# Optimization experiments

Hardware: AMD Instinct MI355X
Metric: run time of the kernel (lower is better)

The kernel has to match this reference:

```python
import jax, jax.numpy as jnp
import numpy as np

N = 50000      # nodes
E = 800000     # edges
DIN = 256
DH = 256
DOUT = 64


def setup_inputs() -> dict:
    key = jax.random.key(0)
    ks = jax.random.split(key, 8)
    x = jax.random.normal(ks[0], (N, DIN), dtype=jnp.float32)
    edge_index = jax.random.randint(ks[1], (2, E), 0, N, dtype=jnp.int64)
    s = 0.05
    W1 = jax.random.normal(ks[2], (DIN, DH), dtype=jnp.float32) * s
    b1 = jnp.zeros((DH,), dtype=jnp.float32)
    W2 = jax.random.normal(ks[3], (DH, DH), dtype=jnp.float32) * s
    b2 = jnp.zeros((DH,), dtype=jnp.float32)
    W3 = jax.random.normal(ks[4], (DH, DOUT), dtype=jnp.float32) * s
    b3 = jnp.zeros((DOUT,), dtype=jnp.float32)
    return {"x": x, "edge_index": edge_index, "W1": W1, "b1": b1,
            "W2": W2, "b2": b2, "W3": W3, "b3": b3}


def gcn_conv(x, src, dst, deg_inv_sqrt, W, b):
    # x: [N, din] -> [N, dout]. PyG GCNConv: h = D^{-1/2}(A+I)D^{-1/2} (x W) + b
    n = x.shape[0]
    h = x @ W                                   # [N, dout]
    norm = deg_inv_sqrt[src] * deg_inv_sqrt[dst]  # [E+N]
    msgs = h[src] * norm[:, None]               # gather + scale, [E+N, dout]
    out = jax.ops.segment_sum(msgs, dst, num_segments=n)  # scatter-add
    return out + b


def _loops(edge_index, n):
    # add self loops, compute symmetric normalization degrees
    sl = jnp.arange(n, dtype=edge_index.dtype)
    src = jnp.concatenate([edge_index[0], sl])
    dst = jnp.concatenate([edge_index[1], sl])
    deg = jax.ops.segment_sum(jnp.ones_like(dst, dtype=jnp.float32), dst, num_segments=n)
    dis = jnp.where(deg > 0, jax.lax.rsqrt(deg), 0.0)
    return src, dst, dis


def reference(x, edge_index, W1, b1, W2, b2, W3, b3):
    src, dst, dis = _loops(edge_index, x.shape[0])
    h = jax.nn.relu(gcn_conv(x, src, dst, dis, W1, b1))   # dropout: eval no-op
    h = jax.nn.relu(gcn_conv(h, src, dst, dis, W2, b2))
    out = gcn_conv(h, src, dst, dis, W3, b3)              # batch=None -> no pooling
    return out
```

## Files before the change

kernel.cpp:

```cpp
#include <hip/hip_runtime.h>
#include <cstdint>
#include <cstddef>

typedef unsigned short u16;
typedef _Float16 f16x8 __attribute__((ext_vector_type(8)));
typedef _Float16 h2 __attribute__((ext_vector_type(2)));
typedef float f32x4 __attribute__((ext_vector_type(4)));

__device__ __forceinline__ float h2f(u16 u) {
  return (float)__builtin_bit_cast(_Float16, u);
}
__device__ __forceinline__ u16 f2h(float f) {
  return __builtin_bit_cast(u16, (_Float16)f);
}

__device__ __forceinline__ void async16(u16* lds, const u16* g) {
  __builtin_amdgcn_global_load_lds(
      (const __attribute__((address_space(1))) unsigned int*)g,
      (__attribute__((address_space(3))) unsigned int*)lds, 16, 0, 0);
}

__device__ __forceinline__ void fma8(float* a, float d, uint4 p) {
  a[0] += d * h2f((u16)p.x); a[1] += d * h2f((u16)(p.x >> 16));
  a[2] += d * h2f((u16)p.y); a[3] += d * h2f((u16)(p.y >> 16));
  a[4] += d * h2f((u16)p.z); a[5] += d * h2f((u16)(p.z >> 16));
  a[6] += d * h2f((u16)p.w); a[7] += d * h2f((u16)(p.w >> 16));
}

__device__ __forceinline__ void pkfma4(h2* acc, h2 w, uint4 p) {
  acc[0] += __builtin_bit_cast(h2, p.x) * w;
  acc[1] += __builtin_bit_cast(h2, p.y) * w;
  acc[2] += __builtin_bit_cast(h2, p.z) * w;
  acc[3] += __builtin_bit_cast(h2, p.w) * w;
}

__device__ __forceinline__ int wave_is64(const void* ep) {
  const unsigned* p = (const unsigned*)ep;
  const int lane = threadIdx.x & 63;
  unsigned v = p[2 * lane + 1] | p[2 * (lane + 64) + 1];
  unsigned long long bal = __ballot(v != 0u);
  return (bal == 0ull) ? 1 : 0;
}

__device__ __forceinline__ int edge_at(const void* ep, int is64, long long idx) {
  if (is64) return (int)((const long long*)ep)[idx];
  return ((const int*)ep)[idx];
}

__global__ void zero_f32(float* p, int n) {
  int i = blockIdx.x * 256 + threadIdx.x;
  if (i < n) p[i] = 0.f;
}

__global__ __launch_bounds__(256) void prep_fused(
    const float4* __restrict__ x, ushort4* __restrict__ xpad, int n_src4, int n_tot4,
    const float* __restrict__ W1, u16* __restrict__ wt1,
    const float* __restrict__ W2, u16* __restrict__ wt2,
    const float* __restrict__ W3, u16* __restrict__ wt3,
    int DIN, int DH, int DOUT,
    int nb_cvt, int nb_w1, int nb_w2) {
  int b = blockIdx.x;
  if (b < nb_cvt) {
    int i = b * 256 + threadIdx.x;
    if (i < n_tot4) {
      ushort4 o = {0, 0, 0, 0};
      if (i < n_src4) {
        float4 v = x[i];
        o.x = f2h(v.x); o.y = f2h(v.y); o.z = f2h(v.z); o.w = f2h(v.w);
      }
      xpad[i] = o;
    }
    return;
  }
  b -= nb_cvt;
  if (b < nb_w1) {
    int idx = b * 256 + threadIdx.x;
    if (idx < DIN * DH) {
      int n = idx / DIN, k = idx % DIN;
      wt1[idx] = f2h(W1[k * DH + n]);
    }
    return;
  }
  b -= nb_w1;
  if (b < nb_w2) {
    int idx = b * 256 + threadIdx.x;
    if (idx < DH * DH) {
      int n = idx / DH, k = idx % DH;
      wt2[idx] = f2h(W2[k * DH + n]);
    }
    return;
  }
  b -= nb_w2;
  {
    int idx = b * 256 + threadIdx.x;
    if (idx < DH * DOUT) {
      int n = idx / DH, k = idx % DH;
      wt3[idx] = f2h(W3[k * DOUT + n]);
    }
  }
}

#define NCHUNK 64

__global__ __launch_bounds__(256) void csr_hist(const void* __restrict__ ep,
                                                int* __restrict__ cnt, int E, int N) {
  __shared__ int h[256];
  h[threadIdx.x] = 0;
  __syncthreads();
  int is64 = wave_is64(ep);
  const int chunk = blockIdx.x;
  const int per = (E + NCHUNK - 1) / NCHUNK;
  const int e0 = chunk * per, e1 = min(e0 + per, E);
  for (int e = e0 + threadIdx.x; e < e1; e += 256) {
    int d = edge_at(ep, is64, (long long)E + e);
    d = min(max(d, 0), N - 1);
    atomicAdd(&h[d >> 8], 1);
  }
  __syncthreads();
  cnt[threadIdx.x * NCHUNK + chunk] = h[threadIdx.x];
}

__global__ __launch_bounds__(256) void csr_base(const int* __restrict__ cnt,
                                                int* __restrict__ bases,
                                                int* __restrict__ off,
                                                int nbuck, int E) {
  __shared__ int ws4[8];
  const int t = threadIdx.x, lane = t & 63, w = t >> 6;
  int tot = 0;
  if (t < nbuck)
#pragma unroll 8
    for (int c = 0; c < NCHUNK; ++c) tot += cnt[t * NCHUNK + c];
  int inc = tot;
#pragma unroll
  for (int o = 1; o < 64; o <<= 1) {
    int u = __shfl_up(inc, o, 64);
    if (lane >= o) inc += u;
  }
  if (lane == 63) ws4[w] = inc;
  __syncthreads();
  if (t == 0) {
    int run = 0;
#pragma unroll
    for (int k = 0; k < 4; ++k) { int v = ws4[k]; ws4[k + 4] = run; run += v; }
  }
  __syncthreads();
  const int base = ws4[w + 4] + inc - tot;
  if (t < nbuck) {
    bases[t] = base;
    int run = base;
    for (int c = 0; c < NCHUNK; ++c) {
      off[t * NCHUNK + c] = run;
      run += cnt[t * NCHUNK + c];
    }
  }
  if (t == 0) bases[nbuck] = E;
}

__global__ __launch_bounds__(256) void csr_bucket(const void* __restrict__ ep,
                                                  const int* __restrict__ off,
                                                  unsigned* __restrict__ tmp,
                                                  int E, int N) {
  __shared__ int cur[256];
  const int chunk = blockIdx.x;
  const int nbuck = (N + 255) >> 8;
  if ((int)threadIdx.x < nbuck) cur[threadIdx.x] = off[threadIdx.x * NCHUNK + chunk];
  __syncthreads();
  int is64 = wave_is64(ep);
  const int per = (E + NCHUNK - 1) / NCHUNK;
  const int e0 = chunk * per, e1 = min(e0 + per, E);
  for (int e = e0 + threadIdx.x; e < e1; e += 256) {
    int s = edge_at(ep, is64, e);
    int d = edge_at(ep, is64, (long long)E + e);
    s = min(max(s, 0), N - 1);
    d = min(max(d, 0), N - 1);
    int pos = atomicAdd(&cur[d >> 8], 1);
    tmp[pos] = ((unsigned)d << 16) | (unsigned)s;
  }
}

__global__ __launch_bounds__(256) void csr_final(const unsigned* __restrict__ tmp,
                                                 const int* __restrict__ bases,
                                                 int* __restrict__ rp,
                                                 float* __restrict__ dis,
                                                 u16* __restrict__ col, int N, int E) {
  __shared__ int hcnt[256];
  __shared__ int curs[256];
  __shared__ int ws4[8];
  const int b = blockIdx.x;
  const int node0 = b * 256;
  const int t = threadIdx.x, lane = t & 63, w = t >> 6;
  hcnt[t] = 0;
  __syncthreads();
  const int k0 = bases[b];
  const int k1 = bases[b + 1];
  for (int k = k0 + t; k < k1; k += 256)
    atomicAdd(&hcnt[(int)(tmp[k] >> 16) - node0], 1);
  __syncthreads();
  const int v = hcnt[t];
  int inc = v;
#pragma unroll
  for (int o = 1; o < 64; o <<= 1) {
    int u = __shfl_up(inc, o, 64);
    if (lane >= o) inc += u;
  }
  if (lane == 63) ws4[w] = inc;
  __syncthreads();
  if (t == 0) {
    int run = 0;
#pragma unroll
    for (int k = 0; k < 4; ++k) { int vv = ws4[k]; ws4[k + 4] = run; run += vv; }
  }
  __syncthreads();
  const int excl = k0 + ws4[w + 4] + inc - v;
  if (node0 + t < N) {
    rp[node0 + t] = excl;
    dis[node0 + t] = rsqrtf((float)(v + 1));
  }
  if (b == 0 && t == 0) rp[N] = E;
  curs[t] = excl;
  __syncthreads();
  for (int k = k0 + t; k < k1; k += 256) {
    unsigned e = tmp[k];
    int dl = (int)(e >> 16) - node0;
    int pos = atomicAdd(&curs[dl], 1);
    col[pos] = (u16)(e & 0xFFFFu);
  }
}

template <int BN>
__global__ __launch_bounds__(256) void gemm_bres(const u16* __restrict__ A,
                                                 const u16* __restrict__ Bt,
                                                 u16* __restrict__ C, int Nt) {
  constexpr int K = 256;
  constexpr int NJ = BN / 16;
  constexpr int CH = BN * K / 8;
  __shared__ __align__(16) u16 Bs[BN * K];

  const int tid = threadIdx.x, lane = tid & 63, w = tid >> 6;
  const int bm = blockIdx.x, bn = blockIdx.y;

#pragma unroll
  for (int i = 0; i < CH / 256; ++i) {
    int c = tid + i * 256;
    int ln = c & 63, t2 = c >> 6;
    int ks = t2 & 7, j = t2 >> 3;
    int row = j * 16 + (ln & 15);
    int kk = ks * 32 + (ln >> 4) * 8;
    async16(&Bs[(size_t)c * 8], Bt + (size_t)(bn * BN + row) * K + kk);
  }

  const int r16 = lane & 15, quad = lane >> 4;
  const int m0 = w * 32;

  const u16* Ap0 = A + (size_t)(bm * 128 + m0 + r16) * K + quad * 8;
  const u16* Ap1 = Ap0 + 16 * K;
  f16x8 aa0[8], aa1[8];
#pragma unroll
  for (int ks = 0; ks < 8; ++ks) {
    aa0[ks] = *(const f16x8*)(Ap0 + ks * 32);
    aa1[ks] = *(const f16x8*)(Ap1 + ks * 32);
  }

  f32x4 acc[2][NJ];
  const f32x4 fzero = {0.f, 0.f, 0.f, 0.f};
#pragma unroll
  for (int i = 0; i < 2; ++i)
#pragma unroll
    for (int j = 0; j < NJ; ++j) acc[i][j] = fzero;

  __syncthreads();

#pragma unroll
  for (int ks = 0; ks < 8; ++ks) {
#pragma unroll
    for (int j = 0; j < NJ; ++j) {
      f16x8 bf = *(const f16x8*)(&Bs[(size_t)((j * 8 + ks) * 64 + lane) * 8]);
      acc[0][j] = __builtin_amdgcn_mfma_f32_16x16x32_f16(aa0[ks], bf, acc[0][j], 0, 0, 0);
      acc[1][j] = __builtin_amdgcn_mfma_f32_16x16x32_f16(aa1[ks], bf, acc[1][j], 0, 0, 0);
    }
  }
#pragma unroll
  for (int i = 0; i < 2; ++i)
#pragma unroll
    for (int j = 0; j < NJ; ++j) {
      int gr = bm * 128 + m0 + i * 16 + quad * 4;
      int gc = bn * BN + j * 16 + r16;
#pragma unroll
      for (int r = 0; r < 4; ++r)
        C[(size_t)(gr + r) * Nt + gc] = f2h(acc[i][j][r]);
    }
}

__global__ __launch_bounds__(256) void agg_d256(const u16* __restrict__ h,
                                                const int* __restrict__ rp,
                                                const u16* __restrict__ col,
                                                const float* __restrict__ dis,
                                                const float* __restrict__ bias,
                                                u16* __restrict__ out, int N) {
  const int wid = threadIdx.x >> 6, lane = threadIdx.x & 63;
  const int i = blockIdx.x * 4 + wid;
  if (i >= N) return;
  const int sub = lane >> 5;
  const int l32 = lane & 31;
  const int c8 = l32 * 8;
  const float di = dis[i];
  h2 acc[4];
  {
    uint4 sv = *(const uint4*)(h + (size_t)i * 256 + c8);
    const _Float16 w = (_Float16)(sub ? 0.f : di);
    const h2 ws = {w, w};
    acc[0] = __builtin_bit_cast(h2, sv.x) * ws;
    acc[1] = __builtin_bit_cast(h2, sv.y) * ws;
    acc[2] = __builtin_bit_cast(h2, sv.z) * ws;
    acc[3] = __builtin_bit_cast(h2, sv.w) * ws;
  }
  const int e1 = rp[i + 1];
  for (int base = rp[i]; base < e1; base += 64) {
    int me = base + lane;
    int s_l = 0; float d_l = 0.f;
    if (me < e1) { s_l = (int)col[me]; d_l = dis[s_l]; }
    const int cnt = min(64, e1 - base);
    const int cntR = (cnt + 7) & ~7;
    for (int t = 0; t < cntR; t += 8) {
      int sA = __shfl(s_l, t + sub, 64);      float dA = __shfl(d_l, t + sub, 64);
      int sB = __shfl(s_l, t + 2 + sub, 64);  float dB = __shfl(d_l, t + 2 + sub, 64);
      int sC = __shfl(s_l, t + 4 + sub, 64);  float dC = __shfl(d_l, t + 4 + sub, 64);
      int sD = __shfl(s_l, t + 6 + sub, 64);  float dD = __shfl(d_l, t + 6 + sub, 64);
      uint4 pA = *(const uint4*)(h + (size_t)sA * 256 + c8);
      uint4 pB = *(const uint4*)(h + (size_t)sB * 256 + c8);
      uint4 pC = *(const uint4*)(h + (size_t)sC * 256 + c8);
      uint4 pD = *(const uint4*)(h + (size_t)sD * 256 + c8);
      _Float16 hA = (_Float16)dA, hB = (_Float16)dB;
      _Float16 hC = (_Float16)dC, hD = (_Float16)dD;
      h2 wA = {hA, hA}, wB = {hB, hB}, wC = {hC, hC}, wD = {hD, hD};
      pkfma4(acc, wA, pA); pkfma4(acc, wB, pB);
      pkfma4(acc, wC, pC); pkfma4(acc, wD, pD);
    }
  }
  float a[8];
#pragma unroll
  for (int j = 0; j < 4; ++j) {
    a[2 * j] = (float)acc[j].x;
    a[2 * j + 1] = (float)acc[j].y;
  }
#pragma unroll
  for (int k = 0; k < 8; ++k) a[k] += __shfl_xor(a[k], 32, 64);
  if (sub == 0) {
    float4 b0 = *(const float4*)(bias + c8);
    float4 b1 = *(const float4*)(bias + c8 + 4);
    float r0 = fmaxf(di * a[0] + b0.x, 0.f), r1 = fmaxf(di * a[1] + b0.y, 0.f);
    float r2 = fmaxf(di * a[2] + b0.z, 0.f), r3 = fmaxf(di * a[3] + b0.w, 0.f);
    float r4 = fmaxf(di * a[4] + b1.x, 0.f), r5 = fmaxf(di * a[5] + b1.y, 0.f);
    float r6 = fmaxf(di * a[6] + b1.z, 0.f), r7 = fmaxf(di * a[7] + b1.w, 0.f);
    uint4 ov;
    ov.x = (unsigned)f2h(r0) | ((unsigned)f2h(r1) << 16);
    ov.y = (unsigned)f2h(r2) | ((unsigned)f2h(r3) << 16);
    ov.z = (unsigned)f2h(r4) | ((unsigned)f2h(r5) << 16);
    ov.w = (unsigned)f2h(r6) | ((unsigned)f2h(r7) << 16);
    *(uint4*)(out + (size_t)i * 256 + c8) = ov;
  }
}

__global__ __launch_bounds__(256) void agg_d64(const u16* __restrict__ h,
                                               const int* __restrict__ rp,
                                               const u16* __restrict__ col,
                                               const float* __restrict__ dis,
                                               const float* __restrict__ bias,
                                               float* __restrict__ out, int N) {
  const int wid = threadIdx.x >> 6, lane = threadIdx.x & 63;
  const int i = blockIdx.x * 4 + wid;
  if (i >= N) return;
  const int grp = lane >> 3;
  const int l8 = lane & 7;
  const int c8 = l8 * 8;
  const float di = dis[i];
  float a[8];
  {
    uint4 sv = *(const uint4*)(h + (size_t)i * 64 + c8);
    const float w = (grp == 0) ? di : 0.f;
    a[0] = w * h2f((u16)sv.x); a[1] = w * h2f((u16)(sv.x >> 16));
    a[2] = w * h2f((u16)sv.y); a[3] = w * h2f((u16)(sv.y >> 16));
    a[4] = w * h2f((u16)sv.z); a[5] = w * h2f((u16)(sv.z >> 16));
    a[6] = w * h2f((u16)sv.w); a[7] = w * h2f((u16)(sv.w >> 16));
  }
  const int e1 = rp[i + 1];
  for (int base = rp[i]; base < e1; base += 64) {
    int me = base + lane;
    int s_l = 0; float d_l = 0.f;
    if (me < e1) { s_l = (int)col[me]; d_l = dis[s_l]; }
    const int cnt = min(64, e1 - base);
    const int cntR = (cnt + 15) & ~15;
    for (int t = 0; t < cntR; t += 16) {
      int sA = __shfl(s_l, t + grp, 64);       float dA = __shfl(d_l, t + grp, 64);
      int sB = __shfl(s_l, t + 8 + grp, 64);   float dB = __shfl(d_l, t + 8 + grp, 64);
      uint4 pA = *(const uint4*)(h + (size_t)sA * 64 + c8);
      uint4 pB = *(const uint4*)(h + (size_t)sB * 64 + c8);
      fma8(a, dA, pA); fma8(a, dB, pB);
    }
  }
#pragma unroll
  for (int k = 0; k < 8; ++k) a[k] += __shfl_xor(a[k], 8, 64);
#pragma unroll
  for (int k = 0; k < 8; ++k) a[k] += __shfl_xor(a[k], 16, 64);
#pragma unroll
  for (int k = 0; k < 8; ++k) a[k] += __shfl_xor(a[k], 32, 64);
  if (lane < 8) {
    float4 b0 = *(const float4*)(bias + c8);
    float4 b1 = *(const float4*)(bias + c8 + 4);
    float4 o0, o1;
    o0.x = di * a[0] + b0.x; o0.y = di * a[1] + b0.y;
    o0.z = di * a[2] + b0.z; o0.w = di * a[3] + b0.w;
    o1.x = di * a[4] + b1.x; o1.y = di * a[5] + b1.y;
    o1.z = di * a[6] + b1.z; o1.w = di * a[7] + b1.w;
    *(float4*)(out + (size_t)i * 64 + c8) = o0;
    *(float4*)(out + (size_t)i * 64 + c8 + 4) = o1;
  }
}

extern "C" void kernel_launch(void* const* d_in, const int* in_sizes, int n_in,
                              void* d_out, int out_size, void* d_ws, size_t ws_size,
                              hipStream_t stream) {
  if (n_in < 8) return;
  const float* x = (const float*)d_in[0];
  const void* eptr = d_in[1];
  const float* W1 = (const float*)d_in[2];
  const float* b1 = (const float*)d_in[3];
  const float* W2 = (const float*)d_in[4];
  const float* b2 = (const float*)d_in[5];
  const float* W3 = (const float*)d_in[6];
  const float* b3 = (const float*)d_in[7];
  float* out = (float*)d_out;

  const int DIN = 256, DH = 256;
  const int N = in_sizes[0] / DIN;
  const int E = in_sizes[1] / 2;
  const int DOUT = in_sizes[6] / DH;
  const int MT = (N + 127) / 128;
  const int Mpad = MT * 128;
  const int nbuck = (N + 255) >> 8;

  auto rnd = [](size_t b) { return (b + 255) & ~(size_t)255; };
  size_t required = 0;
  required += rnd((size_t)Mpad * DH * 2) * 2;
  required += rnd((size_t)E * 2);
  required += rnd((size_t)E * 4);
  required += rnd((size_t)(N + 1) * 4);
  required += rnd((size_t)N * 4);
  required += rnd((size_t)DIN * DH * 2);
  required += rnd((size_t)DH * DH * 2);
  required += rnd((size_t)DH * DOUT * 2);
  required += rnd((size_t)256 * NCHUNK * 4) * 2;
  required += rnd((size_t)(nbuck + 1) * 4);
  if (ws_size < required || N > 65536 || nbuck > 256) {
    zero_f32<<<(out_size + 255) / 256, 256, 0, stream>>>(out, out_size);
    return;
  }

  char* ws = (char*)d_ws;
  size_t off0 = 0;
  auto alloc = [&](size_t bytes) {
    char* p = ws + off0;
    off0 = (off0 + bytes + 255) & ~(size_t)255;
    return p;
  };
  u16* xpad = (u16*)alloc((size_t)Mpad * DH * 2);
  u16* hbuf = (u16*)alloc((size_t)Mpad * DH * 2);
  u16* colb = (u16*)alloc((size_t)E * 2);
  unsigned* tmpb = (unsigned*)alloc((size_t)E * 4);
  int* rp = (int*)alloc((size_t)(N + 1) * 4);
  float* dis = (float*)alloc((size_t)N * 4);
  u16* wt1 = (u16*)alloc((size_t)DIN * DH * 2);
  u16* wt2 = (u16*)alloc((size_t)DH * DH * 2);
  u16* wt3 = (u16*)alloc((size_t)DH * DOUT * 2);
  int* cnt = (int*)alloc((size_t)256 * NCHUNK * 4);
  int* offs = (int*)alloc((size_t)256 * NCHUNK * 4);
  int* bases = (int*)alloc((size_t)(nbuck + 1) * 4);

  const int n_tot4 = Mpad * DH / 4;
  const int nb_cvt = (n_tot4 + 255) / 256;
  const int nb_w1 = (DIN * DH + 255) / 256;
  const int nb_w2 = (DH * DH + 255) / 256;
  const int nb_w3 = (DH * DOUT + 255) / 256;
  prep_fused<<<nb_cvt + nb_w1 + nb_w2 + nb_w3, 256, 0, stream>>>(
      (const float4*)x, (ushort4*)xpad, N * DH / 4, n_tot4,
      W1, wt1, W2, wt2, W3, wt3, DIN, DH, DOUT, nb_cvt, nb_w1, nb_w2);

  csr_hist<<<NCHUNK, 256, 0, stream>>>(eptr, cnt, E, N);
  csr_base<<<1, 256, 0, stream>>>(cnt, bases, offs, nbuck, E);
  csr_bucket<<<NCHUNK, 256, 0, stream>>>(eptr, offs, tmpb, E, N);
  csr_final<<<nbuck, 256, 0, stream>>>(tmpb, bases, rp, dis, colb, N, E);

  gemm_bres<128><<<dim3(MT, DH / 128), 256, 0, stream>>>(xpad, wt1, hbuf, DH);
  agg_d256<<<(N + 3) / 4, 256, 0, stream>>>(hbuf, rp, colb, dis, b1, xpad, N);
  gemm_bres<128><<<dim3(MT, DH / 128), 256, 0, stream>>>(xpad, wt2, hbuf, DH);
  agg_d256<<<(N + 3) / 4, 256, 0, stream>>>(hbuf, rp, colb, dis, b2, xpad, N);
  gemm_bres<64><<<dim3(MT, DOUT / 64), 256, 0, stream>>>(xpad, wt3, hbuf, DOUT);
  agg_d64<<<(N + 3) / 4, 256, 0, stream>>>(hbuf, rp, colb, dis, b3, out, N);
}
```

Baseline: 350.5 us.

## Fuse CSR build into one persistent kernel with global flag barriers

Folds the destination histogram into the prep kernel and merges the base scan, bucketing and final CSR passes into a single kernel that synchronises its blocks through global atomic flags instead of separate launches. This removes three kernel launches and their idle gaps from the small serial CSR phase. It also unrolls the edge loop of the 64-wide aggregation from two to four gathers per iteration to raise memory-level parallelism. The spin-wait barriers assume every block of the CSR grid (max of nbuck and 64, here 196) is resident at once, which can deadlock if that does not hold.

```diff
diff --git a/kernel.cpp b/kernel.cpp
--- a/kernel.cpp
+++ b/kernel.cpp
@@ -47,18 +47,21 @@
   return ((const int*)ep)[idx];
 }
 
+#define NCHUNK 64
+
 __global__ void zero_f32(float* p, int n) {
   int i = blockIdx.x * 256 + threadIdx.x;
   if (i < n) p[i] = 0.f;
 }
 
-__global__ __launch_bounds__(256) void prep_fused(
+__global__ __launch_bounds__(256) void prep_all(
     const float4* __restrict__ x, ushort4* __restrict__ xpad, int n_src4, int n_tot4,
     const float* __restrict__ W1, u16* __restrict__ wt1,
     const float* __restrict__ W2, u16* __restrict__ wt2,
     const float* __restrict__ W3, u16* __restrict__ wt3,
-    int DIN, int DH, int DOUT,
-    int nb_cvt, int nb_w1, int nb_w2) {
+    const void* __restrict__ ep, int* __restrict__ cnt, int* __restrict__ sync,
+    int E, int N, int DIN, int DH, int DOUT,
+    int nb_cvt, int nb_w1, int nb_w2, int nb_w3) {
   int b = blockIdx.x;
   if (b < nb_cvt) {
     int i = b * 256 + threadIdx.x;
@@ -91,138 +94,152 @@
     return;
   }
   b -= nb_w2;
-  {
+  if (b < nb_w3) {
     int idx = b * 256 + threadIdx.x;
     if (idx < DH * DOUT) {
       int n = idx / DH, k = idx % DH;
       wt3[idx] = f2h(W3[k * DOUT + n]);
     }
-  }
-}
-
-#define NCHUNK 64
-
-__global__ __launch_bounds__(256) void csr_hist(const void* __restrict__ ep,
-                                                int* __restrict__ cnt, int E, int N) {
-  __shared__ int h[256];
-  h[threadIdx.x] = 0;
-  __syncthreads();
-  int is64 = wave_is64(ep);
-  const int chunk = blockIdx.x;
-  const int per = (E + NCHUNK - 1) / NCHUNK;
-  const int e0 = chunk * per, e1 = min(e0 + per, E);
-  for (int e = e0 + threadIdx.x; e < e1; e += 256) {
-    int d = edge_at(ep, is64, (long long)E + e);
-    d = min(max(d, 0), N - 1);
-    atomicAdd(&h[d >> 8], 1);
-  }
-  __syncthreads();
-  cnt[threadIdx.x * NCHUNK + chunk] = h[threadIdx.x];
-}
-
-__global__ __launch_bounds__(256) void csr_base(const int* __restrict__ cnt,
-                                                int* __restrict__ bases,
-                                                int* __restrict__ off,
-                                                int nbuck, int E) {
+    return;
+  }
+  b -= nb_w3;
+  if (b < NCHUNK) {
+    __shared__ int h[256];
+    h[threadIdx.x] = 0;
+    __syncthreads();
+    int is64 = wave_is64(ep);
+    const int per = (E + NCHUNK - 1) / NCHUNK;
+    const int e0 = b * per, e1 = min(e0 + per, E);
+    for (int e = e0 + (int)threadIdx.x; e < e1; e += 256) {
+      int d = edge_at(ep, is64, (long long)E + e);
+      d = min(max(d, 0), N - 1);
+      atomicAdd(&h[d >> 8], 1);
+    }
+    __syncthreads();
+    cnt[threadIdx.x * NCHUNK + b] = h[threadIdx.x];
+    return;
+  }
+  b -= NCHUNK;
+  {
+    if (threadIdx.x < 16) sync[threadIdx.x] = 0;
+  }
+}
+
+__global__ __launch_bounds__(256) void csr_all(const void* __restrict__ ep,
+                                               const int* __restrict__ cnt,
+                                               int* __restrict__ bases,
+                                               int* __restrict__ offs,
+                                               unsigned* __restrict__ tmp,
+                                               int* __restrict__ rp,
+                                               float* __restrict__ dis,
+                                               u16* __restrict__ col,
+                                               int* __restrict__ sync,
+                                               int E, int N, int nbuck) {
+  __shared__ int sh[256];
+  __shared__ int sh2[256];
   __shared__ int ws4[8];
-  const int t = threadIdx.x, lane = t & 63, w = t >> 6;
-  int tot = 0;
-  if (t < nbuck)
-#pragma unroll 8
-    for (int c = 0; c < NCHUNK; ++c) tot += cnt[t * NCHUNK + c];
-  int inc = tot;
+  const int b = blockIdx.x, t = threadIdx.x, lane = t & 63, w = t >> 6;
+
+  if (b == 0) {
+    int tot = 0;
+    if (t < nbuck)
+      for (int c = 0; c < NCHUNK; ++c) tot += cnt[t * NCHUNK + c];
+    int inc = tot;
+#pragma unroll
+    for (int o = 1; o < 64; o <<= 1) {
+      int u = __shfl_up(inc, o, 64);
+      if (lane >= o) inc += u;
+    }
+    if (lane == 63) ws4[w] = inc;
+    __syncthreads();
+    if (t == 0) {
+      int run = 0;
+#pragma unroll
+      for (int k = 0; k < 4; ++k) { int v = ws4[k]; ws4[k + 4] = run; run += v; }
+    }
+    __syncthreads();
+    int base = ws4[w + 4] + inc - tot;
+    if (t < nbuck) {
+      bases[t] = base;
+      int run = base;
+      for (int c = 0; c < NCHUNK; ++c) {
+        offs[t * NCHUNK + c] = run;
+        run += cnt[t * NCHUNK + c];
+      }
+    }
+    if (t == 0) bases[nbuck] = E;
+    __threadfence();
+    __syncthreads();
+    if (t == 0)
+      __hip_atomic_store(&sync[0], 1, __ATOMIC_RELEASE, __HIP_MEMORY_SCOPE_AGENT);
+  } else {
+    if (t == 0) {
+      while (__hip_atomic_load(&sync[0], __ATOMIC_ACQUIRE, __HIP_MEMORY_SCOPE_AGENT) == 0)
+        __builtin_amdgcn_s_sleep(8);
+    }
+    __syncthreads();
+  }
+
+  if (b < NCHUNK) {
+    if (t < nbuck) sh[t] = offs[t * NCHUNK + b];
+    __syncthreads();
+    int is64 = wave_is64(ep);
+    const int per = (E + NCHUNK - 1) / NCHUNK;
+    const int e0 = b * per, e1 = min(e0 + per, E);
+    for (int e = e0 + t; e < e1; e += 256) {
+      int s = edge_at(ep, is64, e);
+      int d = edge_at(ep, is64, (long long)E + e);
+      s = min(max(s, 0), N - 1);
+      d = min(max(d, 0), N - 1);
+      int pos = atomicAdd(&sh[d >> 8], 1);
+      tmp[pos] = ((unsigned)d << 16) | (unsigned)s;
+    }
+    __threadfence();
+    __syncthreads();
+    if (t == 0)
+      __hip_atomic_fetch_add(&sync[1], 1, __ATOMIC_RELEASE, __HIP_MEMORY_SCOPE_AGENT);
+  }
+  if (t == 0) {
+    while (__hip_atomic_load(&sync[1], __ATOMIC_ACQUIRE, __HIP_MEMORY_SCOPE_AGENT) < NCHUNK)
+      __builtin_amdgcn_s_sleep(8);
+  }
+  __syncthreads();
+
+  if (b >= nbuck) return;
+  sh[t] = 0;
+  __syncthreads();
+  const int node0 = b * 256;
+  const int k0 = bases[b], k1 = bases[b + 1];
+  for (int k = k0 + t; k < k1; k += 256)
+    atomicAdd(&sh[(int)(tmp[k] >> 16) - node0], 1);
+  __syncthreads();
+  const int v = sh[t];
+  int inc2 = v;
 #pragma unroll
   for (int o = 1; o < 64; o <<= 1) {
-    int u = __shfl_up(inc, o, 64);
-    if (lane >= o) inc += u;
-  }
-  if (lane == 63) ws4[w] = inc;
+    int u = __shfl_up(inc2, o, 64);
+    if (lane >= o) inc2 += u;
+  }
+  if (lane == 63) ws4[w] = inc2;
   __syncthreads();
   if (t == 0) {
     int run = 0;
 #pragma unroll
-    for (int k = 0; k < 4; ++k) { int v = ws4[k]; ws4[k + 4] = run; run += v; }
-  }
-  __syncthreads();
-  const int base = ws4[w + 4] + inc - tot;
-  if (t < nbuck) {
-    bases[t] = base;
-    int run = base;
-    for (int c = 0; c < NCHUNK; ++c) {
-      off[t * NCHUNK + c] = run;
-      run += cnt[t * NCHUNK + c];
-    }
-  }
-  if (t == 0) bases[nbuck] = E;
-}
-
-__global__ __launch_bounds__(256) void csr_bucket(const void* __restrict__ ep,
-                                                  const int* __restrict__ off,
-                                                  unsigned* __restrict__ tmp,
-                                                  int E, int N) {
-  __shared__ int cur[256];
-  const int chunk = blockIdx.x;
-  const int nbuck = (N + 255) >> 8;
-  if ((int)threadIdx.x < nbuck) cur[threadIdx.x] = off[threadIdx.x * NCHUNK + chunk];
-  __syncthreads();
-  int is64 = wave_is64(ep);
-  const int per = (E + NCHUNK - 1) / NCHUNK;
-  const int e0 = chunk * per, e1 = min(e0 + per, E);
-  for (int e = e0 + threadIdx.x; e < e1; e += 256) {
-    int s = edge_at(ep, is64, e);
-    int d = edge_at(ep, is64, (long long)E + e);
-    s = min(max(s, 0), N - 1);
-    d = min(max(d, 0), N - 1);
-    int pos = atomicAdd(&cur[d >> 8], 1);
-    tmp[pos] = ((unsigned)d << 16) | (unsigned)s;
-  }
-}
-
-__global__ __launch_bounds__(256) void csr_final(const unsigned* __restrict__ tmp,
-                                                 const int* __restrict__ bases,
-                                                 int* __restrict__ rp,
-                                                 float* __restrict__ dis,
-                                                 u16* __restrict__ col, int N, int E) {
-  __shared__ int hcnt[256];
-  __shared__ int curs[256];
-  __shared__ int ws4[8];
-  const int b = blockIdx.x;
-  const int node0 = b * 256;
-  const int t = threadIdx.x, lane = t & 63, w = t >> 6;
-  hcnt[t] = 0;
-  __syncthreads();
-  const int k0 = bases[b];
-  const int k1 = bases[b + 1];
-  for (int k = k0 + t; k < k1; k += 256)
-    atomicAdd(&hcnt[(int)(tmp[k] >> 16) - node0], 1);
-  __syncthreads();
-  const int v = hcnt[t];
-  int inc = v;
-#pragma unroll
-  for (int o = 1; o < 64; o <<= 1) {
-    int u = __shfl_up(inc, o, 64);
-    if (lane >= o) inc += u;
-  }
-  if (lane == 63) ws4[w] = inc;
-  __syncthreads();
-  if (t == 0) {
-    int run = 0;
-#pragma unroll
     for (int k = 0; k < 4; ++k) { int vv = ws4[k]; ws4[k + 4] = run; run += vv; }
   }
   __syncthreads();
-  const int excl = k0 + ws4[w + 4] + inc - v;
+  const int excl = k0 + ws4[w + 4] + inc2 - v;
   if (node0 + t < N) {
     rp[node0 + t] = excl;
     dis[node0 + t] = rsqrtf((float)(v + 1));
   }
   if (b == 0 && t == 0) rp[N] = E;
-  curs[t] = excl;
+  sh2[t] = excl;
   __syncthreads();
   for (int k = k0 + t; k < k1; k += 256) {
     unsigned e = tmp[k];
     int dl = (int)(e >> 16) - node0;
-    int pos = atomicAdd(&curs[dl], 1);
+    int pos = atomicAdd(&sh2[dl], 1);
     col[pos] = (u16)(e & 0xFFFFu);
   }
 }
@@ -389,13 +406,17 @@
     int s_l = 0; float d_l = 0.f;
     if (me < e1) { s_l = (int)col[me]; d_l = dis[s_l]; }
     const int cnt = min(64, e1 - base);
-    const int cntR = (cnt + 15) & ~15;
-    for (int t = 0; t < cntR; t += 16) {
+    const int cntR = (cnt + 31) & ~31;
+    for (int t = 0; t < cntR; t += 32) {
       int sA = __shfl(s_l, t + grp, 64);       float dA = __shfl(d_l, t + grp, 64);
       int sB = __shfl(s_l, t + 8 + grp, 64);   float dB = __shfl(d_l, t + 8 + grp, 64);
+      int sC = __shfl(s_l, t + 16 + grp, 64);  float dC = __shfl(d_l, t + 16 + grp, 64);
+      int sD = __shfl(s_l, t + 24 + grp, 64);  float dD = __shfl(d_l, t + 24 + grp, 64);
       uint4 pA = *(const uint4*)(h + (size_t)sA * 64 + c8);
       uint4 pB = *(const uint4*)(h + (size_t)sB * 64 + c8);
-      fma8(a, dA, pA); fma8(a, dB, pB);
+      uint4 pC = *(const uint4*)(h + (size_t)sC * 64 + c8);
+      uint4 pD = *(const uint4*)(h + (size_t)sD * 64 + c8);
+      fma8(a, dA, pA); fma8(a, dB, pB); fma8(a, dC, pC); fma8(a, dD, pD);
     }
   }
 #pragma unroll
@@ -451,7 +472,8 @@
   required += rnd((size_t)DH * DOUT * 2);
   required += rnd((size_t)256 * NCHUNK * 4) * 2;
   required += rnd((size_t)(nbuck + 1) * 4);
-  if (ws_size < required || N > 65536 || nbuck > 256) {
+  required += 256;
+  if (ws_size < required || N > 65536 || nbuck > 256 || nbuck < 1) {
     zero_f32<<<(out_size + 255) / 256, 256, 0, stream>>>(out, out_size);
     return;
   }
@@ -475,20 +497,21 @@
   int* cnt = (int*)alloc((size_t)256 * NCHUNK * 4);
   int* offs = (int*)alloc((size_t)256 * NCHUNK * 4);
   int* bases = (int*)alloc((size_t)(nbuck + 1) * 4);
+  int* syncp = (int*)alloc(256);
 
   const int n_tot4 = Mpad * DH / 4;
   const int nb_cvt = (n_tot4 + 255) / 256;
   const int nb_w1 = (DIN * DH + 255) / 256;
   const int nb_w2 = (DH * DH + 255) / 256;
   const int nb_w3 = (DH * DOUT + 255) / 256;
-  prep_fused<<<nb_cvt + nb_w1 + nb_w2 + nb_w3, 256, 0, stream>>>(
+  prep_all<<<nb_cvt + nb_w1 + nb_w2 + nb_w3 + NCHUNK + 1, 256, 0, stream>>>(
       (const float4*)x, (ushort4*)xpad, N * DH / 4, n_tot4,
-      W1, wt1, W2, wt2, W3, wt3, DIN, DH, DOUT, nb_cvt, nb_w1, nb_w2);
-
-  csr_hist<<<NCHUNK, 256, 0, stream>>>(eptr, cnt, E, N);
-  csr_base<<<1, 256, 0, stream>>>(cnt, bases, offs, nbuck, E);
-  csr_bucket<<<NCHUNK, 256, 0, stream>>>(eptr, offs, tmpb, E, N);
-  csr_final<<<nbuck, 256, 0, stream>>>(tmpb, bases, rp, dis, colb, N, E);
+      W1, wt1, W2, wt2, W3, wt3, eptr, cnt, syncp,
+      E, N, DIN, DH, DOUT, nb_cvt, nb_w1, nb_w2, nb_w3);
+
+  const int gcsr = (nbuck > NCHUNK) ? nbuck : NCHUNK;
+  csr_all<<<gcsr, 256, 0, stream>>>(eptr, cnt, bases, offs, tmpb, rp, dis, colb,
+                                    syncp, E, N, nbuck);
 
   gemm_bres<128><<<dim3(MT, DH / 128), 256, 0, stream>>>(xpad, wt1, hbuf, DH);
   agg_d256<<<(N + 3) / 4, 256, 0, stream>>>(hbuf, rp, colb, dis, b1, xpad, N);
```

Measured after the change: 470.8 us. 34.3% more time.
